# Kernel tuning notes

Hardware: AMD Instinct MI355X
Metric: run time of the kernel (lower is better)

Reference implementation:

```python
import math
import jax, jax.numpy as jnp
import numpy as np

DIM = 512
HEADS = 8
LS = 64  # local_size
SCALE = (DIM // HEADS) ** -0.5


def _normalize(x, eps=1e-12):
    # torch F.normalize(dim=-1): x / max(||x||, eps)
    n = jnp.linalg.norm(x, axis=-1, keepdims=True)
    return x / jnp.maximum(n, eps)


def setup_inputs() -> dict:
    key = jax.random.key(0)
    k0, k1, k2 = jax.random.split(key, 3)
    B, S, D = 8, 4096, DIM
    return {
        "x": jax.random.normal(k0, (B, S, D), jnp.float32),
        "W_qkv": jax.random.normal(k1, (D, 3 * D), jnp.float32) * 0.02,
        "b_qkv": jnp.zeros((3 * D,), jnp.float32),
        "W_proj": jax.random.normal(k2, (D, D), jnp.float32) * 0.02,
        "b_proj": jnp.zeros((D,), jnp.float32),
    }


def reference(x, W_qkv, b_qkv, W_proj, b_proj):
    B, S, D = x.shape
    H = HEADS
    d = D // H
    ls = LS
    nl = S // ls
    ntimes = int(math.log2(nl))

    # qkv projection -> [3, B, H, S, d]
    qkv = (x @ W_qkv + b_qkv).reshape(B, S, 3, H, d).transpose(2, 0, 3, 1, 4)
    q_pre = qkv[0].reshape(B * H, S, d).transpose(0, 2, 1)  # [BH, d, S]

    q_idx_last = jnp.broadcast_to(jnp.arange(S)[None, :], (B * H, S))

    # recursive content-based bipartition (unrolled: ntimes is static)
    for _ in range(ntimes):
        bh, dd, n = q_pre.shape
        q_avg = q_pre.reshape(bh, dd, 2, n // 2).mean(-1)        # [bh, d, 2]
        q_avg = _normalize(q_avg.transpose(0, 2, 1))             # [bh, 2, d]
        q_norm = _normalize(q_pre.transpose(0, 2, 1))            # [bh, n, d]
        # squared euclidean distance [bh, n, 2]
        sq = (jnp.sum(q_norm ** 2, -1)[:, :, None]
              + jnp.sum(q_avg ** 2, -1)[:, None, :]
              - 2.0 * jnp.einsum('bnd,bcd->bnc', q_norm, q_avg))
        q_ratio = (sq[:, :, 0] + 1.0) / (sq[:, :, 1] + 1.0)
        q_idx = jnp.argsort(q_ratio, axis=-1)                    # [bh, n]
        q_idx_last = jnp.take_along_axis(q_idx_last, q_idx, axis=-1).reshape(bh * 2, n // 2)
        q_pre = jnp.take_along_axis(q_pre, q_idx[:, None, :], axis=-1)
        # 'b d (c n) -> (b c) d n' with c=2
        q_pre = q_pre.reshape(bh, dd, 2, n // 2).transpose(0, 2, 1, 3).reshape(bh * 2, dd, n // 2)

    q_idx = q_idx_last.reshape(B, H, S)
    q_idx_rev = jnp.argsort(q_idx, axis=-1)

    # gather qkv along token dim with routed permutation
    qkv_pre = jnp.take_along_axis(qkv, q_idx[None, :, :, :, None], axis=3)  # [3,B,H,S,d]
    # 'qkv b h (nl ls) d -> qkv (b nl) h ls d'
    qkv_pre = qkv_pre.reshape(3, B, H, nl, ls, d).transpose(0, 1, 3, 2, 4, 5).reshape(3, B * nl, H, ls, d)
    q, k, v = qkv_pre[0], qkv_pre[1], qkv_pre[2]

    # windowed diff-softmax-mul attention (softmax over head dim d)
    attn = jax.nn.softmax((q - k) * SCALE, axis=-1)
    out = attn * v                                               # [(B nl), H, ls, d]

    # '(b nl) h ls d -> b h d (nl ls)'
    out = out.reshape(B, nl, H, ls, d).transpose(0, 2, 4, 1, 3).reshape(B, H, d, S)
    out = jnp.take_along_axis(out, q_idx_rev[:, :, None, :], axis=-1)
    res = out.reshape(B, D, S).transpose(0, 2, 1)                # [B, S, D]
    res = res @ W_proj + b_proj
    return x + res
```

## Files before the change

### kernel.cpp

```cpp
#include <hip/hip_runtime.h>
#include <hip/hip_bf16.h>

typedef __bf16 bf16;
typedef __attribute__((ext_vector_type(8))) __bf16 bf16x8;
typedef __attribute__((ext_vector_type(4))) __bf16 bf16x4;
typedef __attribute__((ext_vector_type(4))) float f32x4;

#define M_TOK 32768
#define D_    512
#define N_QKV 1536
#define BK    64
#define SCALE_ 0.125f

#define AS1 __attribute__((address_space(1)))
#define AS3 __attribute__((address_space(3)))

__global__ __launch_bounds__(256) void cvt_bf16(const float* __restrict__ in,
                                                bf16* __restrict__ out, int n4) {
  int i = blockIdx.x * 256 + threadIdx.x;
  if (i >= n4) return;
  f32x4 v = ((const f32x4*)in)[i];
  bf16x4 o;
  o[0] = (bf16)v[0]; o[1] = (bf16)v[1]; o[2] = (bf16)v[2]; o[3] = (bf16)v[3];
  ((bf16x4*)out)[i] = o;
}

template <int PERM>
__global__ __launch_bounds__(256) void transpose_cvt(const float* __restrict__ in,
                                                     bf16* __restrict__ out,
                                                     int K, int N) {
  __shared__ float tile[32][33];
  int n0 = blockIdx.x * 32, k0 = blockIdx.y * 32;
  int tx = threadIdx.x, ty = threadIdx.y;
  for (int i = 0; i < 32; i += 8)
    tile[ty + i][tx] = in[(size_t)(k0 + ty + i) * N + n0 + tx];
  __syncthreads();
  for (int i = 0; i < 32; i += 8) {
    int n = n0 + ty + i;
    int np = n;
    if (PERM) {
      int h = (n & 511) >> 6, qkv = n >> 9;
      np = h * 192 + qkv * 64 + (n & 63);
    }
    out[(size_t)np * K + k0 + tx] = (bf16)tile[tx][ty + i];
  }
}

__global__ __launch_bounds__(256, 2) void gemm_qkv_softmax(const bf16* __restrict__ A,
                                                           const bf16* __restrict__ Bt,
                                                           const float* __restrict__ bqkv,
                                                           bf16* __restrict__ O) {
  __shared__ __align__(16) bf16 sA[2][128 * BK];
  __shared__ __align__(16) bf16 sB[2][192 * BK];

  const int tid = threadIdx.x;
  const int w = tid >> 6;
  const int l = tid & 63;
  const int m0 = blockIdx.x * 128;
  const int h  = blockIdx.y;
  const int n0 = h * 192;

  f32x4 acc[2][12];
#pragma unroll
  for (int i = 0; i < 2; ++i)
#pragma unroll
    for (int j = 0; j < 12; ++j) {
      f32x4 z = {0.f, 0.f, 0.f, 0.f};
      acc[i][j] = z;
    }

  const int srow = l >> 3;
  const int schunk = ((l & 7) ^ (l >> 3)) * 8;

  const int fr = l & 15;
  const int fkc = l >> 4;
  const int frs = fr & 7;

  const bf16* gA = A + (size_t)(m0 + w * 32 + srow) * D_ + schunk;
  const bf16* gB = Bt + (size_t)(n0 + w * 48 + srow) * D_ + schunk;

  auto stageA = [&](int buf, int kt) {
#pragma unroll
    for (int q = 0; q < 4; ++q)
      __builtin_amdgcn_global_load_lds((AS1 const void*)(gA + (size_t)(q * 8) * D_ + kt),
                                       (AS3 void*)&sA[buf][(w * 32 + q * 8) * BK], 16, 0, 0);
  };
  auto stageB = [&](int buf, int kt) {
#pragma unroll
    for (int q = 0; q < 6; ++q)
      __builtin_amdgcn_global_load_lds((AS1 const void*)(gB + (size_t)(q * 8) * D_ + kt),
                                       (AS3 void*)&sB[buf][(w * 48 + q * 8) * BK], 16, 0, 0);
  };

  stageA(0, 0);
  stageB(0, 0);

  const int NT = D_ / BK;
#pragma unroll
  for (int t = 0; t < NT; ++t) {
    const int cur = t & 1;
    if (t < NT - 1) {
      stageA(cur ^ 1, (t + 1) * BK);
      asm volatile("s_waitcnt vmcnt(4)" ::: "memory");
    } else {
      asm volatile("s_waitcnt vmcnt(0)" ::: "memory");
    }
    __builtin_amdgcn_s_barrier();
    asm volatile("" ::: "memory");

    {
      const int sw = (fkc ^ frs) * 8;
      bf16x8 af0 = *(const bf16x8*)&sA[cur][(w * 32 + 0  + fr) * BK + sw];
      bf16x8 af1 = *(const bf16x8*)&sA[cur][(w * 32 + 16 + fr) * BK + sw];
      __builtin_amdgcn_s_setprio(1);
#pragma unroll
      for (int j = 0; j < 12; ++j) {
        bf16x8 bfj = *(const bf16x8*)&sB[cur][(j * 16 + fr) * BK + sw];
        acc[0][j] = __builtin_amdgcn_mfma_f32_16x16x32_bf16(af0, bfj, acc[0][j], 0, 0, 0);
        acc[1][j] = __builtin_amdgcn_mfma_f32_16x16x32_bf16(af1, bfj, acc[1][j], 0, 0, 0);
      }
      __builtin_amdgcn_s_setprio(0);
    }

    if (t < NT - 1) stageB(cur ^ 1, (t + 1) * BK);

    {
      const int sw = ((4 | fkc) ^ frs) * 8;
      bf16x8 af0 = *(const bf16x8*)&sA[cur][(w * 32 + 0  + fr) * BK + sw];
      bf16x8 af1 = *(const bf16x8*)&sA[cur][(w * 32 + 16 + fr) * BK + sw];
      __builtin_amdgcn_s_setprio(1);
#pragma unroll
      for (int j = 0; j < 12; ++j) {
        bf16x8 bfj = *(const bf16x8*)&sB[cur][(j * 16 + fr) * BK + sw];
        acc[0][j] = __builtin_amdgcn_mfma_f32_16x16x32_bf16(af0, bfj, acc[0][j], 0, 0, 0);
        acc[1][j] = __builtin_amdgcn_mfma_f32_16x16x32_bf16(af1, bfj, acc[1][j], 0, 0, 0);
      }
      __builtin_amdgcn_s_setprio(0);
    }
    asm volatile("" ::: "memory");
    __builtin_amdgcn_s_barrier();
  }

  float bq[4], bk[4], bv[4];
#pragma unroll
  for (int jq = 0; jq < 4; ++jq) {
    int c = h * 64 + jq * 16 + fr;
    bq[jq] = bqkv[c];
    bk[jq] = bqkv[512 + c];
    bv[jq] = bqkv[1024 + c];
  }

  const int rbase = (l >> 4) * 4;
#pragma unroll
  for (int i = 0; i < 2; ++i) {
#pragma unroll
    for (int r = 0; r < 4; ++r) {
      float sc[4];
#pragma unroll
      for (int jq = 0; jq < 4; ++jq)
        sc[jq] = (acc[i][jq][r] + bq[jq] - acc[i][jq + 4][r] - bk[jq]) * SCALE_;
      float mx = fmaxf(fmaxf(sc[0], sc[1]), fmaxf(sc[2], sc[3]));
#pragma unroll
      for (int off = 1; off < 16; off <<= 1) mx = fmaxf(mx, __shfl_xor(mx, off));
      float e[4];
      float sum = 0.f;
#pragma unroll
      for (int jq = 0; jq < 4; ++jq) { e[jq] = __expf(sc[jq] - mx); sum += e[jq]; }
#pragma unroll
      for (int off = 1; off < 16; off <<= 1) sum += __shfl_xor(sum, off);
      float inv = 1.0f / sum;
      int m = m0 + w * 32 + i * 16 + rbase + r;
#pragma unroll
      for (int jq = 0; jq < 4; ++jq) {
        float o = e[jq] * inv * (acc[i][jq + 8][r] + bv[jq]);
        O[(size_t)m * D_ + h * 64 + jq * 16 + fr] = (bf16)o;
      }
    }
  }
}

__global__ __launch_bounds__(256, 2) void gemm_bt_f32(const bf16* __restrict__ A,
                                                      const bf16* __restrict__ Bt,
                                                      const float* __restrict__ bias,
                                                      const float* __restrict__ resid,
                                                      float* __restrict__ C,
                                                      int M, int N, int K) {
  __shared__ __align__(16) bf16 sA[2][128 * BK];
  __shared__ __align__(16) bf16 sB[2][128 * BK];

  const int tid = threadIdx.x;
  const int w = tid >> 6;
  const int l = tid & 63;
  const int m0 = blockIdx.x * 128;
  const int n0 = blockIdx.y * 128;
  const int wrow = w >> 1, wcol = w & 1;

  f32x4 acc[4][4];
#pragma unroll
  for (int i = 0; i < 4; ++i)
#pragma unroll
    for (int j = 0; j < 4; ++j) {
      f32x4 z = {0.f, 0.f, 0.f, 0.f};
      acc[i][j] = z;
    }

  const int srow = l >> 3;
  const int schunk = ((l & 7) ^ (l >> 3)) * 8;
  const int fr = l & 15;
  const int fkc = l >> 4;
  const int frs = fr & 7;

  const bf16* gA = A + (size_t)(m0 + w * 32 + srow) * K + schunk;
  const bf16* gB = Bt + (size_t)(n0 + w * 32 + srow) * K + schunk;

  auto stageA = [&](int buf, int kt) {
#pragma unroll
    for (int q = 0; q < 4; ++q)
      __builtin_amdgcn_global_load_lds((AS1 const void*)(gA + (size_t)(q * 8) * K + kt),
                                       (AS3 void*)&sA[buf][(w * 32 + q * 8) * BK], 16, 0, 0);
  };
  auto stageB = [&](int buf, int kt) {
#pragma unroll
    for (int q = 0; q < 4; ++q)
      __builtin_amdgcn_global_load_lds((AS1 const void*)(gB + (size_t)(q * 8) * K + kt),
                                       (AS3 void*)&sB[buf][(w * 32 + q * 8) * BK], 16, 0, 0);
  };

  stageA(0, 0);
  stageB(0, 0);

  const int nt = K / BK;
  for (int t = 0; t < nt; ++t) {
    const int cur = t & 1;
    if (t < nt - 1) {
      stageA(cur ^ 1, (t + 1) * BK);
      asm volatile("s_waitcnt vmcnt(4)" ::: "memory");
    } else {
      asm volatile("s_waitcnt vmcnt(0)" ::: "memory");
    }
    __builtin_amdgcn_s_barrier();
    asm volatile("" ::: "memory");

    {
      const int sw = (fkc ^ frs) * 8;
      bf16x8 af[4], bfr[4];
#pragma unroll
      for (int i = 0; i < 4; ++i)
        af[i] = *(const bf16x8*)&sA[cur][(wrow * 64 + i * 16 + fr) * BK + sw];
#pragma unroll
      for (int j = 0; j < 4; ++j)
        bfr[j] = *(const bf16x8*)&sB[cur][(wcol * 64 + j * 16 + fr) * BK + sw];
      __builtin_amdgcn_s_setprio(1);
#pragma unroll
      for (int i = 0; i < 4; ++i)
#pragma unroll
        for (int j = 0; j < 4; ++j)
          acc[i][j] = __builtin_amdgcn_mfma_f32_16x16x32_bf16(af[i], bfr[j], acc[i][j], 0, 0, 0);
      __builtin_amdgcn_s_setprio(0);
    }

    if (t < nt - 1) stageB(cur ^ 1, (t + 1) * BK);

    {
      const int sw = ((4 | fkc) ^ frs) * 8;
      bf16x8 af[4], bfr[4];
#pragma unroll
      for (int i = 0; i < 4; ++i)
        af[i] = *(const bf16x8*)&sA[cur][(wrow * 64 + i * 16 + fr) * BK + sw];
#pragma unroll
      for (int j = 0; j < 4; ++j)
        bfr[j] = *(const bf16x8*)&sB[cur][(wcol * 64 + j * 16 + fr) * BK + sw];
      __builtin_amdgcn_s_setprio(1);
#pragma unroll
      for (int i = 0; i < 4; ++i)
#pragma unroll
        for (int j = 0; j < 4; ++j)
          acc[i][j] = __builtin_amdgcn_mfma_f32_16x16x32_bf16(af[i], bfr[j], acc[i][j], 0, 0, 0);
      __builtin_amdgcn_s_setprio(0);
    }
    asm volatile("" ::: "memory");
    __builtin_amdgcn_s_barrier();
  }

  const int col = l & 15;
  const int rbase = (l >> 4) * 4;
#pragma unroll
  for (int j = 0; j < 4; ++j) {
    int n = n0 + wcol * 64 + j * 16 + col;
    float bv = bias[n];
#pragma unroll
    for (int i = 0; i < 4; ++i) {
#pragma unroll
      for (int r = 0; r < 4; ++r) {
        int m = m0 + wrow * 64 + i * 16 + rbase + r;
        C[(size_t)m * N + n] = acc[i][j][r] + bv + resid[(size_t)m * N + n];
      }
    }
  }
}

extern "C" void kernel_launch(void* const* d_in, const int* in_sizes, int n_in,
                              void* d_out, int out_size, void* d_ws, size_t ws_size,
                              hipStream_t stream) {
  const float* x     = (const float*)d_in[0];
  const float* Wqkv  = (const float*)d_in[1];
  const float* bqkv  = (const float*)d_in[2];
  const float* Wproj = (const float*)d_in[3];
  const float* bproj = (const float*)d_in[4];
  float* out = (float*)d_out;

  char* ws = (char*)d_ws;
  bf16* Wq_t = (bf16*)ws;
  bf16* Wp_t = (bf16*)(ws + (size_t)N_QKV * D_ * 2);
  char* p = ws + (size_t)N_QKV * D_ * 2 + (size_t)D_ * D_ * 2;
  bf16* Xb = (bf16*)p;
  bf16* O  = (bf16*)(p + (size_t)M_TOK * D_ * 2);

  transpose_cvt<1><<<dim3(N_QKV / 32, D_ / 32), dim3(32, 8), 0, stream>>>(Wqkv, Wq_t, D_, N_QKV);
  transpose_cvt<0><<<dim3(D_ / 32, D_ / 32), dim3(32, 8), 0, stream>>>(Wproj, Wp_t, D_, D_);

  cvt_bf16<<<(M_TOK * D_ / 4 + 255) / 256, 256, 0, stream>>>(x, Xb, M_TOK * D_ / 4);

  gemm_qkv_softmax<<<dim3(M_TOK / 128, 8), 256, 0, stream>>>(Xb, Wq_t, bqkv, O);

  gemm_bt_f32<<<dim3(M_TOK / 128, D_ / 128), 256, 0, stream>>>(
      O, Wp_t, bproj, x, out, M_TOK, D_, D_);
}
```

Measured before the change: 226.5 us.

## Retile fused QKV GEMM to 2x2 warp grid with cross-warp softmax merge

Changes the QKV GEMM warp layout from each warp owning 32 rows by all 192 columns to a 2x2 warp grid with 64 rows by 96 columns per warp. This reuses each A fragment across more MFMAs and cuts LDS fragment reads per MFMA. To keep the fused softmax correct, the weight columns are permuted so each column-half holds half of q, k and v, and the two halves' max and sum are merged through shared memory. It also peels the last K iteration in both GEMMs to remove branches. The cost is an extra LDS exchange and barrier in the epilogue and more live accumulator registers.

```diff
diff --git a/kernel.cpp b/kernel.cpp
--- a/kernel.cpp
+++ b/kernel.cpp
@@ -39,8 +39,8 @@
     int n = n0 + ty + i;
     int np = n;
     if (PERM) {
-      int h = (n & 511) >> 6, qkv = n >> 9;
-      np = h * 192 + qkv * 64 + (n & 63);
+      int qkv = n >> 9, h = (n & 511) >> 6, c = n & 63;
+      np = h * 192 + (c >> 5) * 96 + qkv * 32 + (c & 31);
     }
     out[(size_t)np * K + k0 + tx] = (bf16)tile[tx][ty + i];
   }
@@ -59,12 +59,13 @@
   const int m0 = blockIdx.x * 128;
   const int h  = blockIdx.y;
   const int n0 = h * 192;
-
-  f32x4 acc[2][12];
-#pragma unroll
-  for (int i = 0; i < 2; ++i)
-#pragma unroll
-    for (int j = 0; j < 12; ++j) {
+  const int wrow = w >> 1, wcol = w & 1;
+
+  f32x4 acc[4][6];
+#pragma unroll
+  for (int i = 0; i < 4; ++i)
+#pragma unroll
+    for (int j = 0; j < 6; ++j) {
       f32x4 z = {0.f, 0.f, 0.f, 0.f};
       acc[i][j] = z;
     }
@@ -92,89 +93,110 @@
                                        (AS3 void*)&sB[buf][(w * 48 + q * 8) * BK], 16, 0, 0);
   };
 
+  auto compute = [&](int buf, int kk) {
+    const int sw = (((kk << 2) | fkc) ^ frs) * 8;
+    bf16x8 af[4], bfr[6];
+#pragma unroll
+    for (int i = 0; i < 4; ++i)
+      af[i] = *(const bf16x8*)&sA[buf][(wrow * 64 + i * 16 + fr) * BK + sw];
+#pragma unroll
+    for (int j = 0; j < 6; ++j)
+      bfr[j] = *(const bf16x8*)&sB[buf][(wcol * 96 + j * 16 + fr) * BK + sw];
+    __builtin_amdgcn_s_setprio(1);
+#pragma unroll
+    for (int i = 0; i < 4; ++i)
+#pragma unroll
+      for (int j = 0; j < 6; ++j)
+        acc[i][j] = __builtin_amdgcn_mfma_f32_16x16x32_bf16(af[i], bfr[j], acc[i][j], 0, 0, 0);
+    __builtin_amdgcn_s_setprio(0);
+  };
+
   stageA(0, 0);
   stageB(0, 0);
 
   const int NT = D_ / BK;
-#pragma unroll
-  for (int t = 0; t < NT; ++t) {
+  for (int t = 0; t < NT - 1; ++t) {
     const int cur = t & 1;
-    if (t < NT - 1) {
-      stageA(cur ^ 1, (t + 1) * BK);
-      asm volatile("s_waitcnt vmcnt(4)" ::: "memory");
-    } else {
-      asm volatile("s_waitcnt vmcnt(0)" ::: "memory");
-    }
-    __builtin_amdgcn_s_barrier();
-    asm volatile("" ::: "memory");
-
-    {
-      const int sw = (fkc ^ frs) * 8;
-      bf16x8 af0 = *(const bf16x8*)&sA[cur][(w * 32 + 0  + fr) * BK + sw];
-      bf16x8 af1 = *(const bf16x8*)&sA[cur][(w * 32 + 16 + fr) * BK + sw];
-      __builtin_amdgcn_s_setprio(1);
-#pragma unroll
-      for (int j = 0; j < 12; ++j) {
-        bf16x8 bfj = *(const bf16x8*)&sB[cur][(j * 16 + fr) * BK + sw];
-        acc[0][j] = __builtin_amdgcn_mfma_f32_16x16x32_bf16(af0, bfj, acc[0][j], 0, 0, 0);
-        acc[1][j] = __builtin_amdgcn_mfma_f32_16x16x32_bf16(af1, bfj, acc[1][j], 0, 0, 0);
+    stageA(cur ^ 1, (t + 1) * BK);
+    asm volatile("s_waitcnt vmcnt(4)" ::: "memory");
+    __builtin_amdgcn_s_barrier();
+    asm volatile("" ::: "memory");
+    compute(cur, 0);
+    stageB(cur ^ 1, (t + 1) * BK);
+    compute(cur, 1);
+    asm volatile("" ::: "memory");
+    __builtin_amdgcn_s_barrier();
+  }
+  {
+    const int cur = (NT - 1) & 1;
+    asm volatile("s_waitcnt vmcnt(0)" ::: "memory");
+    __builtin_amdgcn_s_barrier();
+    asm volatile("" ::: "memory");
+    compute(cur, 0);
+    compute(cur, 1);
+    asm volatile("" ::: "memory");
+    __builtin_amdgcn_s_barrier();
+  }
+
+  float bq[2], bkk[2], bv[2];
+#pragma unroll
+  for (int jq = 0; jq < 2; ++jq) {
+    int c = h * 64 + wcol * 32 + jq * 16 + fr;
+    bq[jq]  = bqkv[c];
+    bkk[jq] = bqkv[512 + c];
+    bv[jq]  = bqkv[1024 + c];
+  }
+
+  float* xm = (float*)&sA[0][0];
+  float* xs = xm + 256;
+  const int rbase = (l >> 4) * 4;
+
+  float mpart[4][4], spart[4][4];
+#pragma unroll
+  for (int i = 0; i < 4; ++i) {
+#pragma unroll
+    for (int r = 0; r < 4; ++r) {
+      float s0 = (acc[i][0][r] + bq[0] - acc[i][2][r] - bkk[0]) * SCALE_;
+      float s1 = (acc[i][1][r] + bq[1] - acc[i][3][r] - bkk[1]) * SCALE_;
+      float mx = fmaxf(s0, s1);
+#pragma unroll
+      for (int off = 1; off < 16; off <<= 1) mx = fmaxf(mx, __shfl_xor(mx, off));
+      float e0 = __expf(s0 - mx);
+      float e1 = __expf(s1 - mx);
+      acc[i][0][r] = e0;
+      acc[i][1][r] = e1;
+      float sm = e0 + e1;
+#pragma unroll
+      for (int off = 1; off < 16; off <<= 1) sm += __shfl_xor(sm, off);
+      mpart[i][r] = mx;
+      spart[i][r] = sm;
+      if (fr == 0) {
+        int row = wrow * 64 + i * 16 + rbase + r;
+        xm[wcol * 128 + row] = mx;
+        xs[wcol * 128 + row] = sm;
       }
-      __builtin_amdgcn_s_setprio(0);
-    }
-
-    if (t < NT - 1) stageB(cur ^ 1, (t + 1) * BK);
-
-    {
-      const int sw = ((4 | fkc) ^ frs) * 8;
-      bf16x8 af0 = *(const bf16x8*)&sA[cur][(w * 32 + 0  + fr) * BK + sw];
-      bf16x8 af1 = *(const bf16x8*)&sA[cur][(w * 32 + 16 + fr) * BK + sw];
-      __builtin_amdgcn_s_setprio(1);
-#pragma unroll
-      for (int j = 0; j < 12; ++j) {
-        bf16x8 bfj = *(const bf16x8*)&sB[cur][(j * 16 + fr) * BK + sw];
-        acc[0][j] = __builtin_amdgcn_mfma_f32_16x16x32_bf16(af0, bfj, acc[0][j], 0, 0, 0);
-        acc[1][j] = __builtin_amdgcn_mfma_f32_16x16x32_bf16(af1, bfj, acc[1][j], 0, 0, 0);
-      }
-      __builtin_amdgcn_s_setprio(0);
-    }
-    asm volatile("" ::: "memory");
-    __builtin_amdgcn_s_barrier();
-  }
-
-  float bq[4], bk[4], bv[4];
-#pragma unroll
-  for (int jq = 0; jq < 4; ++jq) {
-    int c = h * 64 + jq * 16 + fr;
-    bq[jq] = bqkv[c];
-    bk[jq] = bqkv[512 + c];
-    bv[jq] = bqkv[1024 + c];
-  }
-
-  const int rbase = (l >> 4) * 4;
-#pragma unroll
-  for (int i = 0; i < 2; ++i) {
+    }
+  }
+  __syncthreads();
+
+#pragma unroll
+  for (int i = 0; i < 4; ++i) {
 #pragma unroll
     for (int r = 0; r < 4; ++r) {
-      float sc[4];
-#pragma unroll
-      for (int jq = 0; jq < 4; ++jq)
-        sc[jq] = (acc[i][jq][r] + bq[jq] - acc[i][jq + 4][r] - bk[jq]) * SCALE_;
-      float mx = fmaxf(fmaxf(sc[0], sc[1]), fmaxf(sc[2], sc[3]));
-#pragma unroll
-      for (int off = 1; off < 16; off <<= 1) mx = fmaxf(mx, __shfl_xor(mx, off));
-      float e[4];
-      float sum = 0.f;
-#pragma unroll
-      for (int jq = 0; jq < 4; ++jq) { e[jq] = __expf(sc[jq] - mx); sum += e[jq]; }
-#pragma unroll
-      for (int off = 1; off < 16; off <<= 1) sum += __shfl_xor(sum, off);
-      float inv = 1.0f / sum;
-      int m = m0 + w * 32 + i * 16 + rbase + r;
-#pragma unroll
-      for (int jq = 0; jq < 4; ++jq) {
-        float o = e[jq] * inv * (acc[i][jq + 8][r] + bv[jq]);
-        O[(size_t)m * D_ + h * 64 + jq * 16 + fr] = (bf16)o;
-      }
+      int row = wrow * 64 + i * 16 + rbase + r;
+      float mo = xm[(wcol ^ 1) * 128 + row];
+      float so = xs[(wcol ^ 1) * 128 + row];
+      float mx = mpart[i][r];
+      float M  = fmaxf(mx, mo);
+      float esc_self  = __expf(mx - M);
+      float esc_other = __expf(mo - M);
+      float total = spart[i][r] * esc_self + so * esc_other;
+      float inv = esc_self / total;
+      int m = m0 + row;
+      float o0 = acc[i][0][r] * inv * (acc[i][4][r] + bv[0]);
+      float o1 = acc[i][1][r] * inv * (acc[i][5][r] + bv[1]);
+      O[(size_t)m * D_ + h * 64 + wcol * 32 + fr]      = (bf16)o0;
+      O[(size_t)m * D_ + h * 64 + wcol * 32 + 16 + fr] = (bf16)o1;
     }
   }
 }
@@ -226,60 +248,47 @@
                                        (AS3 void*)&sB[buf][(w * 32 + q * 8) * BK], 16, 0, 0);
   };
 
+  auto compute = [&](int buf, int kk) {
+    const int sw = (((kk << 2) | fkc) ^ frs) * 8;
+    bf16x8 af[4], bfr[4];
+#pragma unroll
+    for (int i = 0; i < 4; ++i)
+      af[i] = *(const bf16x8*)&sA[buf][(wrow * 64 + i * 16 + fr) * BK + sw];
+#pragma unroll
+    for (int j = 0; j < 4; ++j)
+      bfr[j] = *(const bf16x8*)&sB[buf][(wcol * 64 + j * 16 + fr) * BK + sw];
+    __builtin_amdgcn_s_setprio(1);
+#pragma unroll
+    for (int i = 0; i < 4; ++i)
+#pragma unroll
+      for (int j = 0; j < 4; ++j)
+        acc[i][j] = __builtin_amdgcn_mfma_f32_16x16x32_bf16(af[i], bfr[j], acc[i][j], 0, 0, 0);
+    __builtin_amdgcn_s_setprio(0);
+  };
+
   stageA(0, 0);
   stageB(0, 0);
 
   const int nt = K / BK;
-  for (int t = 0; t < nt; ++t) {
+  for (int t = 0; t < nt - 1; ++t) {
     const int cur = t & 1;
-    if (t < nt - 1) {
-      stageA(cur ^ 1, (t + 1) * BK);
-      asm volatile("s_waitcnt vmcnt(4)" ::: "memory");
-    } else {
-      asm volatile("s_waitcnt vmcnt(0)" ::: "memory");
-    }
-    __builtin_amdgcn_s_barrier();
-    asm volatile("" ::: "memory");
-
-    {
-      const int sw = (fkc ^ frs) * 8;
-      bf16x8 af[4], bfr[4];
-#pragma unroll
-      for (int i = 0; i < 4; ++i)
-        af[i] = *(const bf16x8*)&sA[cur][(wrow * 64 + i * 16 + fr) * BK + sw];
-#pragma unroll
-      for (int j = 0; j < 4; ++j)
-        bfr[j] = *(const bf16x8*)&sB[cur][(wcol * 64 + j * 16 + fr) * BK + sw];
-      __builtin_amdgcn_s_setprio(1);
-#pragma unroll
-      for (int i = 0; i < 4; ++i)
-#pragma unroll
-        for (int j = 0; j < 4; ++j)
-          acc[i][j] = __builtin_amdgcn_mfma_f32_16x16x32_bf16(af[i], bfr[j], acc[i][j], 0, 0, 0);
-      __builtin_amdgcn_s_setprio(0);
-    }
-
-    if (t < nt - 1) stageB(cur ^ 1, (t + 1) * BK);
-
-    {
-      const int sw = ((4 | fkc) ^ frs) * 8;
-      bf16x8 af[4], bfr[4];
-#pragma unroll
-      for (int i = 0; i < 4; ++i)
-        af[i] = *(const bf16x8*)&sA[cur][(wrow * 64 + i * 16 + fr) * BK + sw];
-#pragma unroll
-      for (int j = 0; j < 4; ++j)
-        bfr[j] = *(const bf16x8*)&sB[cur][(wcol * 64 + j * 16 + fr) * BK + sw];
-      __builtin_amdgcn_s_setprio(1);
-#pragma unroll
-      for (int i = 0; i < 4; ++i)
-#pragma unroll
-        for (int j = 0; j < 4; ++j)
-          acc[i][j] = __builtin_amdgcn_mfma_f32_16x16x32_bf16(af[i], bfr[j], acc[i][j], 0, 0, 0);
-      __builtin_amdgcn_s_setprio(0);
-    }
-    asm volatile("" ::: "memory");
-    __builtin_amdgcn_s_barrier();
+    stageA(cur ^ 1, (t + 1) * BK);
+    asm volatile("s_waitcnt vmcnt(4)" ::: "memory");
+    __builtin_amdgcn_s_barrier();
+    asm volatile("" ::: "memory");
+    compute(cur, 0);
+    stageB(cur ^ 1, (t + 1) * BK);
+    compute(cur, 1);
+    asm volatile("" ::: "memory");
+    __builtin_amdgcn_s_barrier();
+  }
+  {
+    const int cur = (nt - 1) & 1;
+    asm volatile("s_waitcnt vmcnt(0)" ::: "memory");
+    __builtin_amdgcn_s_barrier();
+    asm volatile("" ::: "memory");
+    compute(cur, 0);
+    compute(cur, 1);
   }
 
   const int col = l & 15;
```

Result: slower. 238.2 us (+5.2%).
